# Kernel tuning notes

Hardware: AMD Instinct MI355X
Metric: run time of the kernel (lower is better)

Reference implementation:

```python
import jax, jax.numpy as jnp
import numpy as np

TOP_N = 5


def _pairwise_euclidean(q, c):
    # q: (b, s, d), c: (b, n, d) -> (b, s, n); matches torch.cdist(p=2)
    q2 = jnp.sum(q * q, axis=-1)[..., None]          # (b, s, 1)
    c2 = jnp.sum(c * c, axis=-1)[:, None, :]         # (b, 1, n)
    qc = jnp.einsum('bsd,bnd->bsn', q, c)            # (b, s, n)
    return jnp.sqrt(jnp.clip(q2 + c2 - 2.0 * qc, 0.0))


def setup_inputs() -> dict:
    key = jax.random.key(0)
    ks = jax.random.split(key, 5)
    b, s, n, d = 4, 2048, 4096, 256
    return {
        'query_embeddings': jax.random.normal(ks[0], (b, s, d), jnp.float32),
        'context_embeddings': jax.random.normal(ks[1], (b, n, d), jnp.float32),
        'memory_embeddings': jax.random.normal(ks[2], (b, n, d), jnp.float32),
        'Wq': jax.random.normal(ks[3], (d, d), jnp.float32) / np.sqrt(d),
        'bq': jnp.zeros((d,), jnp.float32),
        'wg': jax.random.normal(ks[4], (d,), jnp.float32) / np.sqrt(d),
        'bg': jnp.zeros((1,), jnp.float32),
    }


def reference(query_embeddings, context_embeddings, memory_embeddings, Wq, bq, wg, bg):
    # latent query projection (nn.Linear)
    qp = jnp.einsum('bsd,ed->bse', query_embeddings, Wq) + bq  # Wq stored as (out, in)
    dist_ctx = _pairwise_euclidean(qp, context_embeddings)     # (b, s, n)
    dist_mem = _pairwise_euclidean(qp, memory_embeddings)      # (b, s, n)
    # gated fusion of context vs memory distances
    gate = jax.nn.sigmoid(jnp.einsum('bsd,d->bs', query_embeddings, wg) + bg)[..., None]
    distances = dist_ctx * gate + dist_mem * (1.0 - gate)
    # top-n SMALLEST distances
    neg_vals, idx = jax.lax.top_k(-distances, TOP_N)
    return (-neg_vals, idx)
```

## Files before the change

### kernel.cpp

```cpp
#include <hip/hip_runtime.h>
#include <math.h>

#define BB 4
#define SS 2048
#define NN 4096
#define DD 256
#define ROWS (BB*SS)
#define TOPN 5
#define BM 128
#define BN 64
#define BK 64
#define NRB (ROWS/BM)
#define NCBK (NN/BN)
#define NWG (NRB*NCBK)
#define NCAND 16

typedef short bf16x8 __attribute__((ext_vector_type(8)));
typedef float f32x4  __attribute__((ext_vector_type(4)));
typedef unsigned short u16x4 __attribute__((ext_vector_type(4)));

__device__ inline unsigned short f2bf(float f) {
    unsigned int u = __float_as_uint(f);
    unsigned int r = u + 0x7fffu + ((u >> 16) & 1u);
    return (unsigned short)(r >> 16);
}

__device__ inline unsigned pk2h(float a, float b) {
    typedef __fp16 h2 __attribute__((ext_vector_type(2)));
    h2 h = __builtin_amdgcn_cvt_pkrtz(a, b);
    return __builtin_bit_cast(unsigned, h);
}

__device__ inline void gload_lds16(const void* g, void* l) {
    __builtin_amdgcn_global_load_lds(
        (const __attribute__((address_space(1))) unsigned int*)g,
        (__attribute__((address_space(3))) unsigned int*)l, 16, 0, 0);
}

#define INS5A(vv, gg)                                                   \
    do {                                                                \
        unsigned _v = (vv); int _g = (gg);                              \
        if (_v < B4) {                                                  \
            if (_v < B3) { B4 = B3; I4 = I3;                            \
                if (_v < B2) { B3 = B2; I3 = I2;                        \
                    if (_v < B1) { B2 = B1; I2 = I1;                    \
                        if (_v < B0) { B1 = B0; I1 = I0; B0 = _v; I0 = _g; } \
                        else         { B1 = _v; I1 = _g; }              \
                    } else { B2 = _v; I2 = _g; }                        \
                } else { B3 = _v; I3 = _g; }                            \
            } else { B4 = _v; I4 = _g; }                                \
        }                                                               \
    } while (0)

#define INS5B(vv, gg)                                                   \
    do {                                                                \
        unsigned _v = (vv); int _g = (gg);                              \
        if (_v < C4) {                                                  \
            if (_v < C3) { C4 = C3; J4 = J3;                            \
                if (_v < C2) { C3 = C2; J3 = J2;                        \
                    if (_v < C1) { C2 = C1; J2 = J1;                    \
                        if (_v < C0) { C1 = C0; J1 = J0; C0 = _v; J0 = _g; } \
                        else         { C1 = _v; J1 = _g; }              \
                    } else { C2 = _v; J2 = _g; }                        \
                } else { C3 = _v; J3 = _g; }                            \
            } else { C4 = _v; J4 = _g; }                                \
        }                                                               \
    } while (0)

__global__ __launch_bounds__(256) void k_proj64(
    const float* __restrict__ q, const float* __restrict__ Wq,
    const float* __restrict__ bq, double* __restrict__ qp64,
    unsigned short* __restrict__ qpb)
{
    __shared__ float As[64][65];
    __shared__ float Bs[64][65];
    const int rowbase = blockIdx.x * 64;
    const int ebase   = blockIdx.y * 64;
    const int t  = threadIdx.x;
    const int tx = t & 15;
    const int ty = t >> 4;

    double acc[4][4];
    #pragma unroll
    for (int i = 0; i < 4; ++i)
        #pragma unroll
        for (int j = 0; j < 4; ++j) acc[i][j] = 0.0;

    for (int k0 = 0; k0 < DD; k0 += 64) {
        #pragma unroll
        for (int i = 0; i < 4; ++i) {
            int r = ty + (i << 4);
            float4 va = *(const float4*)(q  + (size_t)(rowbase + r) * DD + k0 + (tx << 2));
            As[(tx<<2)+0][r] = va.x; As[(tx<<2)+1][r] = va.y;
            As[(tx<<2)+2][r] = va.z; As[(tx<<2)+3][r] = va.w;
            float4 vb = *(const float4*)(Wq + (size_t)(ebase + r) * DD + k0 + (tx << 2));
            Bs[(tx<<2)+0][r] = vb.x; Bs[(tx<<2)+1][r] = vb.y;
            Bs[(tx<<2)+2][r] = vb.z; Bs[(tx<<2)+3][r] = vb.w;
        }
        __syncthreads();
        #pragma unroll 4
        for (int kk = 0; kk < 64; ++kk) {
            double a[4], bb[4];
            #pragma unroll
            for (int i = 0; i < 4; ++i) a[i]  = (double)As[kk][(ty<<2)+i];
            #pragma unroll
            for (int j = 0; j < 4; ++j) bb[j] = (double)Bs[kk][(tx<<2)+j];
            #pragma unroll
            for (int i = 0; i < 4; ++i)
                #pragma unroll
                for (int j = 0; j < 4; ++j)
                    acc[i][j] = fma(a[i], bb[j], acc[i][j]);
        }
        __syncthreads();
    }
    #pragma unroll
    for (int i = 0; i < 4; ++i) {
        int row = rowbase + (ty << 2) + i;
        #pragma unroll
        for (int j = 0; j < 4; ++j) {
            int e = ebase + (tx << 2) + j;
            double r = acc[i][j] + (double)bq[e];
            qp64[(size_t)row * DD + e] = r;
            qpb[(size_t)row * DD + e] = f2bf((float)r);
        }
    }
}

__global__ __launch_bounds__(256) void k_prep_cm(
    const float* __restrict__ x, unsigned short* __restrict__ xb,
    double* __restrict__ n64, float* __restrict__ n32)
{
    int row  = blockIdx.x * 4 + (threadIdx.x >> 6);
    int lane = threadIdx.x & 63;
    float4 v = *(const float4*)(x + (size_t)row * DD + (lane << 2));
    u16x4 o;
    o[0] = f2bf(v.x); o[1] = f2bf(v.y); o[2] = f2bf(v.z); o[3] = f2bf(v.w);
    *(u16x4*)(xb + (size_t)row * DD + (lane << 2)) = o;
    double s = (double)v.x*(double)v.x + (double)v.y*(double)v.y
             + (double)v.z*(double)v.z + (double)v.w*(double)v.w;
    #pragma unroll
    for (int off = 32; off; off >>= 1) s += __shfl_xor(s, off);
    if (lane == 0) { n64[row] = s; n32[row] = (float)s; }
}

__global__ __launch_bounds__(256) void k_rownorm_d(
    const double* __restrict__ x, double* __restrict__ o64,
    float* __restrict__ o32)
{
    int row  = blockIdx.x * 4 + (threadIdx.x >> 6);
    int lane = threadIdx.x & 63;
    const double* p = x + (size_t)row * DD + (lane << 2);
    double s = p[0]*p[0] + p[1]*p[1] + p[2]*p[2] + p[3]*p[3];
    #pragma unroll
    for (int off = 32; off; off >>= 1) s += __shfl_xor(s, off);
    if (lane == 0) { o64[row] = s; o32[row] = (float)s; }
}

__global__ __launch_bounds__(256) void k_gate(
    const float* __restrict__ q, const float* __restrict__ wg,
    const float* __restrict__ bg, double* __restrict__ g64,
    float* __restrict__ g32)
{
    int row  = blockIdx.x * 4 + (threadIdx.x >> 6);
    int lane = threadIdx.x & 63;
    float4 v = *(const float4*)(q  + (size_t)row * DD + (lane << 2));
    float4 w = *(const float4*)(wg + (lane << 2));
    double s = (double)v.x*(double)w.x + (double)v.y*(double)w.y
             + (double)v.z*(double)w.z + (double)v.w*(double)w.w;
    #pragma unroll
    for (int off = 32; off; off >>= 1) s += __shfl_xor(s, off);
    if (lane == 0) {
        double g = 1.0 / (1.0 + exp(-(s + (double)bg[0])));
        g64[row] = g; g32[row] = (float)g;
    }
}

__global__ __launch_bounds__(256, 1) void k_dist_mfma(
    const unsigned short* __restrict__ qpb,
    const unsigned short* __restrict__ ctxb,
    const unsigned short* __restrict__ memb,
    const float* __restrict__ q2, const float* __restrict__ gate,
    const float* __restrict__ c2c, const float* __restrict__ c2m,
    unsigned* __restrict__ distP)
{
    __shared__ __attribute__((aligned(16))) char smem[32768];
    const int tid  = threadIdx.x;
    const int lane = tid & 63;
    const int wid  = tid >> 6;
    const int wr   = wid >> 1;
    const int wc   = wid & 1;
    const int orig = blockIdx.x;
    const int lid  = (orig & 7) * (NWG / 8) + (orig >> 3);
    const int rowbase = (lid >> 6) * BM;
    const int colbase = (lid & 63) * BN;
    const int b = rowbase / SS;
    const unsigned short* cb  = ctxb + (size_t)b * NN * DD;
    const unsigned short* mbp = memb + (size_t)b * NN * DD;

    f32x4 accC[4][2], accM[4][2];
    f32x4 zz = {0.f, 0.f, 0.f, 0.f};
    #pragma unroll
    for (int i = 0; i < 4; ++i)
        #pragma unroll
        for (int j = 0; j < 2; ++j) { accC[i][j] = zz; accM[i][j] = zz; }

    for (int t = 0; t < DD / BK; ++t) {
        const int k0 = t * BK;
        __syncthreads();
        #pragma unroll
        for (int i = 0; i < 4; ++i) {
            int s = i * 256 + tid;
            int r = s >> 3, c = s & 7;
            const unsigned short* ga = qpb + (size_t)(rowbase + r) * DD + k0 + c * 8;
            gload_lds16(ga, smem + i * 4096 + wid * 1024);
        }
        #pragma unroll
        for (int i = 0; i < 2; ++i) {
            int s = i * 256 + tid;
            int r = s >> 3, c = s & 7;
            const unsigned short* gc = cb  + (size_t)(colbase + r) * DD + k0 + c * 8;
            const unsigned short* gm = mbp + (size_t)(colbase + r) * DD + k0 + c * 8;
            gload_lds16(gc, smem + 16384 + i * 4096 + wid * 1024);
            gload_lds16(gm, smem + 24576 + i * 4096 + wid * 1024);
        }
        __syncthreads();
        #pragma unroll
        for (int ks = 0; ks < 2; ++ks) {
            bf16x8 af[4], bcf[2], bmf[2];
            const int koff = (ks * 4 + (lane >> 4)) * 16;
            #pragma unroll
            for (int f = 0; f < 4; ++f) {
                int arow = wr * 64 + f * 16 + (lane & 15);
                af[f] = *(const bf16x8*)(smem + arow * 128 + koff);
            }
            #pragma unroll
            for (int f = 0; f < 2; ++f) {
                int brow = wc * 32 + f * 16 + (lane & 15);
                bcf[f] = *(const bf16x8*)(smem + 16384 + brow * 128 + koff);
                bmf[f] = *(const bf16x8*)(smem + 24576 + brow * 128 + koff);
            }
            #pragma unroll
            for (int mf = 0; mf < 4; ++mf)
                #pragma unroll
                for (int nf = 0; nf < 2; ++nf) {
                    accC[mf][nf] = __builtin_amdgcn_mfma_f32_16x16x32_bf16(
                        af[mf], bcf[nf], accC[mf][nf], 0, 0, 0);
                    accM[mf][nf] = __builtin_amdgcn_mfma_f32_16x16x32_bf16(
                        af[mf], bmf[nf], accM[mf][nf], 0, 0, 0);
                }
        }
    }

    float q2r[4][4], gr[4][4];
    #pragma unroll
    for (int mf = 0; mf < 4; ++mf)
        #pragma unroll
        for (int rg = 0; rg < 4; ++rg) {
            int r = rowbase + wr * 64 + mf * 16 + ((lane >> 4) << 2) + rg;
            q2r[mf][rg] = q2[r];
            gr[mf][rg]  = gate[r];
        }
    float ccv[2], cmv[2];
    #pragma unroll
    for (int nf = 0; nf < 2; ++nf) {
        int c = colbase + wc * 32 + nf * 16 + (lane & 15);
        ccv[nf] = c2c[b * NN + c];
        cmv[nf] = c2m[b * NN + c];
    }

    #pragma unroll
    for (int mf = 0; mf < 4; ++mf) {
        size_t p0 = (size_t)((rowbase + wr * 64 + mf * 16
                              + ((lane >> 4) << 2)) >> 1) * NN;
        #pragma unroll
        for (int nf = 0; nf < 2; ++nf) {
            int col = colbase + wc * 32 + nf * 16 + (lane & 15);
            float d[4];
            #pragma unroll
            for (int rg = 0; rg < 4; ++rg) {
                float g  = gr[mf][rg];
                float dc = sqrtf(fmaxf(q2r[mf][rg] + ccv[nf]
                                       - 2.0f * accC[mf][nf][rg], 0.f));
                float dm = sqrtf(fmaxf(q2r[mf][rg] + cmv[nf]
                                       - 2.0f * accM[mf][nf][rg], 0.f));
                d[rg] = fmaf(g, dc - dm, dm);
            }
            distP[p0 + col]      = pk2h(d[0], d[1]);
            distP[p0 + NN + col] = pk2h(d[2], d[3]);
        }
    }
}

__global__ __launch_bounds__(256) void k_filter(
    const unsigned* __restrict__ distP, int* __restrict__ cand)
{
    int pair = blockIdx.x * 4 + (threadIdx.x >> 6);
    int lane = threadIdx.x & 63;
    const unsigned* dr = distP + (size_t)pair * NN;

    unsigned B0 = 0xFFFFu, B1 = 0xFFFFu, B2 = 0xFFFFu, B3 = 0xFFFFu, B4 = 0xFFFFu;
    int I0 = 0x7fffffff, I1 = 0x7fffffff, I2 = 0x7fffffff, I3 = 0x7fffffff, I4 = 0x7fffffff;
    unsigned C0 = 0xFFFFu, C1 = 0xFFFFu, C2 = 0xFFFFu, C3 = 0xFFFFu, C4 = 0xFFFFu;
    int J0 = 0x7fffffff, J1 = 0x7fffffff, J2 = 0x7fffffff, J3 = 0x7fffffff, J4 = 0x7fffffff;

    #pragma unroll
    for (int ch = 0; ch < 16; ++ch) {
        uint4 w = *(const uint4*)(dr + ch * 256 + lane * 4);
        int base = ch * 256 + lane * 4;
        INS5A(w.x & 0xFFFFu, base + 0);  INS5B(w.x >> 16, base + 0);
        INS5A(w.y & 0xFFFFu, base + 1);  INS5B(w.y >> 16, base + 1);
        INS5A(w.z & 0xFFFFu, base + 2);  INS5B(w.z >> 16, base + 2);
        INS5A(w.w & 0xFFFFu, base + 3);  INS5B(w.w >> 16, base + 3);
    }

    #pragma unroll
    for (int r = 0; r < NCAND; ++r) {
        unsigned mv = B0; int mi = I0;
        #pragma unroll
        for (int off = 1; off < 64; off <<= 1) {
            unsigned ov = __shfl_xor(mv, off);
            int      oi = __shfl_xor(mi, off);
            if (ov < mv || (ov == mv && oi < mi)) { mv = ov; mi = oi; }
        }
        if (B0 == mv && I0 == mi) {
            B0 = B1; I0 = I1; B1 = B2; I1 = I2; B2 = B3; I2 = I3;
            B3 = B4; I3 = I4; B4 = 0xFFFFu; I4 = 0x7fffffff;
        }
        if (lane == 0) cand[(size_t)(2 * pair) * NCAND + r] = mi;
    }
    #pragma unroll
    for (int r = 0; r < NCAND; ++r) {
        unsigned mv = C0; int mi = J0;
        #pragma unroll
        for (int off = 1; off < 64; off <<= 1) {
            unsigned ov = __shfl_xor(mv, off);
            int      oi = __shfl_xor(mi, off);
            if (ov < mv || (ov == mv && oi < mi)) { mv = ov; mi = oi; }
        }
        if (C0 == mv && J0 == mi) {
            C0 = C1; J0 = J1; C1 = C2; J1 = J2; C2 = C3; J2 = J3;
            C3 = C4; J3 = J4; C4 = 0xFFFFu; J4 = 0x7fffffff;
        }
        if (lane == 0) cand[(size_t)(2 * pair + 1) * NCAND + r] = mi;
    }
}

__global__ __launch_bounds__(256) void k_rescore(
    const double* __restrict__ qp64, const float* __restrict__ ctx,
    const float* __restrict__ mem, const double* __restrict__ q2,
    const double* __restrict__ gate, const double* __restrict__ c2c,
    const double* __restrict__ c2m, const int* __restrict__ cand,
    float* __restrict__ out)
{
    __shared__ double sval[4][NCAND];
    __shared__ int    sidx[4][NCAND];
    const int w    = threadIdx.x >> 6;
    const int row  = blockIdx.x * 4 + w;
    const int lane = threadIdx.x & 63;
    const int b = row / SS;

    const double* qr = qp64 + (size_t)row * DD + (lane << 2);
    double a0 = qr[0], a1 = qr[1], a2 = qr[2], a3 = qr[3];
    double q2r = q2[row], g = gate[row];

    for (int c = 0; c < NCAND; ++c) {
        int idx = cand[(size_t)row * NCAND + c];
        const float4 vc = *(const float4*)(ctx + ((size_t)b * NN + idx) * DD + (lane << 2));
        const float4 vm = *(const float4*)(mem + ((size_t)b * NN + idx) * DD + (lane << 2));
        double sc = a0*(double)vc.x + a1*(double)vc.y + a2*(double)vc.z + a3*(double)vc.w;
        double sm = a0*(double)vm.x + a1*(double)vm.y + a2*(double)vm.z + a3*(double)vm.w;
        #pragma unroll
        for (int off = 32; off; off >>= 1) {
            sc += __shfl_xor(sc, off);
            sm += __shfl_xor(sm, off);
        }
        if (lane == 0) {
            double dc = sqrt(fmax(q2r + c2c[(size_t)b * NN + idx] - 2.0 * sc, 0.0));
            double dm = sqrt(fmax(q2r + c2m[(size_t)b * NN + idx] - 2.0 * sm, 0.0));
            sval[w][c] = g * dc + (1.0 - g) * dm;
            sidx[w][c] = idx;
        }
    }
    if (lane == 0) {
        #pragma unroll
        for (int r = 0; r < TOPN; ++r) {
            double bv = sval[w][0]; int bi = sidx[w][0]; int bp = 0;
            for (int c = 1; c < NCAND; ++c) {
                double v = sval[w][c]; int ii = sidx[w][c];
                if (v < bv || (v == bv && ii < bi)) { bv = v; bi = ii; bp = c; }
            }
            sval[w][bp] = INFINITY; sidx[w][bp] = 0x7fffffff;
            out[(size_t)row * TOPN + r] = (float)bv;
            out[(size_t)ROWS * TOPN + (size_t)row * TOPN + r] = (float)bi;
        }
    }
}

extern "C" void kernel_launch(void* const* d_in, const int* in_sizes, int n_in,
                              void* d_out, int out_size, void* d_ws, size_t ws_size,
                              hipStream_t stream)
{
    const float* q   = (const float*)d_in[0];
    const float* ctx = (const float*)d_in[1];
    const float* mem = (const float*)d_in[2];
    const float* Wq  = (const float*)d_in[3];
    const float* bq  = (const float*)d_in[4];
    const float* wg  = (const float*)d_in[5];
    const float* bg  = (const float*)d_in[6];
    float* out = (float*)d_out;

    char* ws = (char*)d_ws;
    double* qp64  = (double*)ws;  ws += (size_t)ROWS * DD * 8;
    double* q264  = (double*)ws;  ws += (size_t)ROWS * 8;
    double* g64   = (double*)ws;  ws += (size_t)ROWS * 8;
    double* c2c64 = (double*)ws;  ws += (size_t)BB * NN * 8;
    double* c2m64 = (double*)ws;  ws += (size_t)BB * NN * 8;
    unsigned short* qpb  = (unsigned short*)ws; ws += (size_t)ROWS * DD * 2;
    unsigned short* ctxb = (unsigned short*)ws; ws += (size_t)BB * NN * DD * 2;
    unsigned short* memb = (unsigned short*)ws; ws += (size_t)BB * NN * DD * 2;
    float*  q232  = (float*)ws;   ws += (size_t)ROWS * 4;
    float*  g32   = (float*)ws;   ws += (size_t)ROWS * 4;
    float*  c2c32 = (float*)ws;   ws += (size_t)BB * NN * 4;
    float*  c2m32 = (float*)ws;   ws += (size_t)BB * NN * 4;
    unsigned* distP = (unsigned*)ws; ws += (size_t)(ROWS / 2) * NN * 4;
    int*    cand  = (int*)ws;     ws += (size_t)ROWS * NCAND * 4;

    k_proj64<<<dim3(ROWS/64, DD/64), 256, 0, stream>>>(q, Wq, bq, qp64, qpb);
    k_prep_cm<<<(BB*NN)/4, 256, 0, stream>>>(ctx, ctxb, c2c64, c2c32);
    k_prep_cm<<<(BB*NN)/4, 256, 0, stream>>>(mem, memb, c2m64, c2m32);
    k_rownorm_d<<<ROWS/4, 256, 0, stream>>>(qp64, q264, q232);
    k_gate<<<ROWS/4, 256, 0, stream>>>(q, wg, bg, g64, g32);
    k_dist_mfma<<<NWG, 256, 0, stream>>>(
        qpb, ctxb, memb, q232, g32, c2c32, c2m32, distP);
    k_filter<<<(ROWS/2)/4, 256, 0, stream>>>(distP, cand);
    k_rescore<<<ROWS/4, 256, 0, stream>>>(qp64, ctx, mem, q264, g64,
                                          c2c64, c2m64, cand, out);
}
```

Baseline: 225.6 us.

## Merge prep kernels and prune rescore candidates by half-precision distance threshold

Merges the two context/memory prep launches into one, and the q-norm and gate kernels into one row-stats kernel, removing launches. The filter now also stores each candidate's fp16 distance, and rescore stops at the first candidate whose approximate distance exceeds the 5th-best plus a small margin. This cuts fp64 gather-dot work in rescore. The fixed 4-ulp margin could drop a true top-5 element if the fp16/bf16 error exceeds it.

```diff
diff --git a/kernel.cpp b/kernel.cpp
--- a/kernel.cpp
+++ b/kernel.cpp
@@ -126,12 +126,18 @@
     }
 }
 
-__global__ __launch_bounds__(256) void k_prep_cm(
-    const float* __restrict__ x, unsigned short* __restrict__ xb,
-    double* __restrict__ n64, float* __restrict__ n32)
-{
-    int row  = blockIdx.x * 4 + (threadIdx.x >> 6);
+__global__ __launch_bounds__(256) void k_prep_cm2(
+    const float* __restrict__ ctx, const float* __restrict__ mem,
+    unsigned short* __restrict__ ctxb, unsigned short* __restrict__ memb,
+    double* __restrict__ c2c64, double* __restrict__ c2m64,
+    float* __restrict__ c2c32, float* __restrict__ c2m32)
+{
+    int rid  = blockIdx.x * 4 + (threadIdx.x >> 6);
     int lane = threadIdx.x & 63;
+    const float* x; unsigned short* xb; double* n64; float* n32; int row;
+    if (rid < BB * NN) { x = ctx; xb = ctxb; n64 = c2c64; n32 = c2c32; row = rid; }
+    else               { x = mem; xb = memb; n64 = c2m64; n32 = c2m32; row = rid - BB * NN; }
+
     float4 v = *(const float4*)(x + (size_t)row * DD + (lane << 2));
     u16x4 o;
     o[0] = f2bf(v.x); o[1] = f2bf(v.y); o[2] = f2bf(v.z); o[3] = f2bf(v.w);
@@ -143,34 +149,28 @@
     if (lane == 0) { n64[row] = s; n32[row] = (float)s; }
 }
 
-__global__ __launch_bounds__(256) void k_rownorm_d(
-    const double* __restrict__ x, double* __restrict__ o64,
-    float* __restrict__ o32)
+__global__ __launch_bounds__(256) void k_row_stats(
+    const double* __restrict__ qp64, const float* __restrict__ q,
+    const float* __restrict__ wg, const float* __restrict__ bg,
+    double* __restrict__ q264, float* __restrict__ q232,
+    double* __restrict__ g64, float* __restrict__ g32)
 {
     int row  = blockIdx.x * 4 + (threadIdx.x >> 6);
     int lane = threadIdx.x & 63;
-    const double* p = x + (size_t)row * DD + (lane << 2);
+    const double* p = qp64 + (size_t)row * DD + (lane << 2);
     double s = p[0]*p[0] + p[1]*p[1] + p[2]*p[2] + p[3]*p[3];
-    #pragma unroll
-    for (int off = 32; off; off >>= 1) s += __shfl_xor(s, off);
-    if (lane == 0) { o64[row] = s; o32[row] = (float)s; }
-}
-
-__global__ __launch_bounds__(256) void k_gate(
-    const float* __restrict__ q, const float* __restrict__ wg,
-    const float* __restrict__ bg, double* __restrict__ g64,
-    float* __restrict__ g32)
-{
-    int row  = blockIdx.x * 4 + (threadIdx.x >> 6);
-    int lane = threadIdx.x & 63;
     float4 v = *(const float4*)(q  + (size_t)row * DD + (lane << 2));
     float4 w = *(const float4*)(wg + (lane << 2));
-    double s = (double)v.x*(double)w.x + (double)v.y*(double)w.y
+    double t = (double)v.x*(double)w.x + (double)v.y*(double)w.y
              + (double)v.z*(double)w.z + (double)v.w*(double)w.w;
     #pragma unroll
-    for (int off = 32; off; off >>= 1) s += __shfl_xor(s, off);
+    for (int off = 32; off; off >>= 1) {
+        s += __shfl_xor(s, off);
+        t += __shfl_xor(t, off);
+    }
     if (lane == 0) {
-        double g = 1.0 / (1.0 + exp(-(s + (double)bg[0])));
+        q264[row] = s; q232[row] = (float)s;
+        double g = 1.0 / (1.0 + exp(-(t + (double)bg[0])));
         g64[row] = g; g32[row] = (float)g;
     }
 }
@@ -292,7 +292,8 @@
 }
 
 __global__ __launch_bounds__(256) void k_filter(
-    const unsigned* __restrict__ distP, int* __restrict__ cand)
+    const unsigned* __restrict__ distP, int* __restrict__ cand,
+    unsigned short* __restrict__ cval)
 {
     int pair = blockIdx.x * 4 + (threadIdx.x >> 6);
     int lane = threadIdx.x & 63;
@@ -326,7 +327,10 @@
             B0 = B1; I0 = I1; B1 = B2; I1 = I2; B2 = B3; I2 = I3;
             B3 = B4; I3 = I4; B4 = 0xFFFFu; I4 = 0x7fffffff;
         }
-        if (lane == 0) cand[(size_t)(2 * pair) * NCAND + r] = mi;
+        if (lane == 0) {
+            cand[(size_t)(2 * pair) * NCAND + r] = mi;
+            cval[(size_t)(2 * pair) * NCAND + r] = (unsigned short)mv;
+        }
     }
     #pragma unroll
     for (int r = 0; r < NCAND; ++r) {
@@ -341,7 +345,10 @@
             C0 = C1; J0 = J1; C1 = C2; J1 = J2; C2 = C3; J2 = J3;
             C3 = C4; J3 = J4; C4 = 0xFFFFu; J4 = 0x7fffffff;
         }
-        if (lane == 0) cand[(size_t)(2 * pair + 1) * NCAND + r] = mi;
+        if (lane == 0) {
+            cand[(size_t)(2 * pair + 1) * NCAND + r] = mi;
+            cval[(size_t)(2 * pair + 1) * NCAND + r] = (unsigned short)mv;
+        }
     }
 }
 
@@ -350,7 +357,7 @@
     const float* __restrict__ mem, const double* __restrict__ q2,
     const double* __restrict__ gate, const double* __restrict__ c2c,
     const double* __restrict__ c2m, const int* __restrict__ cand,
-    float* __restrict__ out)
+    const unsigned short* __restrict__ cval, float* __restrict__ out)
 {
     __shared__ double sval[4][NCAND];
     __shared__ int    sidx[4][NCAND];
@@ -363,7 +370,15 @@
     double a0 = qr[0], a1 = qr[1], a2 = qr[2], a3 = qr[3];
     double q2r = q2[row], g = gate[row];
 
+    if (lane == 0) {
+        #pragma unroll
+        for (int c = 0; c < NCAND; ++c) { sval[w][c] = INFINITY; sidx[w][c] = 0x7fffffff; }
+    }
+    const unsigned short* cv = cval + (size_t)row * NCAND;
+    const unsigned thresh = (unsigned)cv[4] + 4;
+
     for (int c = 0; c < NCAND; ++c) {
+        if ((unsigned)cv[c] > thresh) break;
         int idx = cand[(size_t)row * NCAND + c];
         const float4 vc = *(const float4*)(ctx + ((size_t)b * NN + idx) * DD + (lane << 2));
         const float4 vm = *(const float4*)(mem + ((size_t)b * NN + idx) * DD + (lane << 2));
@@ -424,15 +439,16 @@
     float*  c2m32 = (float*)ws;   ws += (size_t)BB * NN * 4;
     unsigned* distP = (unsigned*)ws; ws += (size_t)(ROWS / 2) * NN * 4;
     int*    cand  = (int*)ws;     ws += (size_t)ROWS * NCAND * 4;
+    unsigned short* cval = (unsigned short*)ws; ws += (size_t)ROWS * NCAND * 2;
 
     k_proj64<<<dim3(ROWS/64, DD/64), 256, 0, stream>>>(q, Wq, bq, qp64, qpb);
-    k_prep_cm<<<(BB*NN)/4, 256, 0, stream>>>(ctx, ctxb, c2c64, c2c32);
-    k_prep_cm<<<(BB*NN)/4, 256, 0, stream>>>(mem, memb, c2m64, c2m32);
-    k_rownorm_d<<<ROWS/4, 256, 0, stream>>>(qp64, q264, q232);
-    k_gate<<<ROWS/4, 256, 0, stream>>>(q, wg, bg, g64, g32);
+    k_prep_cm2<<<(2*BB*NN)/4, 256, 0, stream>>>(ctx, mem, ctxb, memb,
+                                                c2c64, c2m64, c2c32, c2m32);
+    k_row_stats<<<ROWS/4, 256, 0, stream>>>(qp64, q, wg, bg,
+                                            q264, q232, g64, g32);
     k_dist_mfma<<<NWG, 256, 0, stream>>>(
         qpb, ctxb, memb, q232, g32, c2c32, c2m32, distP);
-    k_filter<<<(ROWS/2)/4, 256, 0, stream>>>(distP, cand);
+    k_filter<<<(ROWS/2)/4, 256, 0, stream>>>(distP, cand, cval);
     k_rescore<<<ROWS/4, 256, 0, stream>>>(qp64, ctx, mem, q264, g64,
-                                          c2c64, c2m64, cand, out);
-}
+                                          c2c64, c2m64, cand, cval, out);
+}
```

New measurement: 206.6 us. 8.4% less time.
